# Kernel optimization log

Hardware: AMD Instinct MI355X
Metric: run time of the kernel (lower is better)

Reference implementation:

```python
import jax, jax.numpy as jnp
import numpy as np

B = 64          # graphs per batch
NP = 512        # nodes per graph (equal-sized graphs)
N = B * NP      # total nodes
E = 1_048_576   # total edges (avg degree 32)
F_IN, H, K, OUT = 16, 128, 2, 2
BN_EPS = 1e-5
EPS = 1e-15


def setup_inputs() -> dict:
    key = jax.random.key(0)
    ks = jax.random.split(key, 12)
    node_feature = jax.random.normal(ks[0], (N, F_IN), jnp.float32)
    # edges constrained to stay within each graph of NP nodes
    g = jax.random.randint(ks[1], (E,), 0, B)
    src = g * NP + jax.random.randint(ks[2], (E,), 0, NP)
    dst = g * NP + jax.random.randint(ks[3], (E,), 0, NP)
    edge_index = jnp.stack([src, dst]).astype(jnp.int32)
    edge_feature = jax.random.uniform(ks[4], (E, 1), jnp.float32)
    batch = (jnp.arange(N, dtype=jnp.int32) // NP)

    def lin(k, i, o):
        return (jax.random.normal(k, (i, o), jnp.float32) / np.sqrt(i)).astype(jnp.float32)

    params = dict(
        W_pre=lin(ks[5], F_IN, H), b_pre=jnp.zeros((H,), jnp.float32),
        W1_rel=lin(ks[6], H, H), b1_rel=jnp.zeros((H,), jnp.float32), W1_root=lin(ks[7], H, H),
        g1=jnp.ones((H,), jnp.float32), be1=jnp.zeros((H,), jnp.float32),
        W2_rel=lin(ks[8], H, H), b2_rel=jnp.zeros((H,), jnp.float32), W2_root=lin(ks[9], H, H),
        g2=jnp.ones((H,), jnp.float32), be2=jnp.zeros((H,), jnp.float32),
        W_pool=lin(ks[10], H, K), b_pool=jnp.zeros((K,), jnp.float32),
        W_post=lin(ks[11], 2 * H, OUT), b_post=jnp.zeros((OUT,), jnp.float32),
    )
    return dict(node_feature=node_feature, edge_index=edge_index,
                edge_feature=edge_feature, batch=batch, **params)


def _graph_conv(x, src, dst, ew, W_rel, b_rel, W_root):
    # PyG GraphConv: out = lin_rel(sum_{j->i} w_e * x_j) + lin_root(x_i)
    msg = x[src] * ew                       # [E, H] gather + scale
    agg = jnp.zeros_like(x).at[dst].add(msg)  # scatter-add to targets
    return agg @ W_rel + b_rel + x @ W_root


def _bn(x, g, b):
    # BatchNorm1d in training mode: batch statistics over nodes (biased var)
    mu = x.mean(0)
    var = jnp.mean((x - mu) ** 2, axis=0)
    return (x - mu) * jax.lax.rsqrt(var + BN_EPS) * g + b


def reference(node_feature, edge_index, edge_feature, batch,
              W_pre, b_pre, W1_rel, b1_rel, W1_root, g1, be1,
              W2_rel, b2_rel, W2_root, g2, be2,
              W_pool, b_pool, W_post, b_post):
    src, dst = edge_index[0], edge_index[1]
    x = node_feature @ W_pre + b_pre
    x = jax.nn.relu(_bn(_graph_conv(x, src, dst, edge_feature, W1_rel, b1_rel, W1_root), g1, be1))
    x = jax.nn.relu(_bn(_graph_conv(x, src, dst, edge_feature, W2_rel, b2_rel, W2_root), g2, be2))
    # dropout p=0.0 -> identity

    # to_dense_batch: equal-sized sorted graphs -> reshape; mask is all-ones
    xd = x.reshape(B, NP, H)
    # to_dense_adj: scatter edge weights into [B, NP, NP]
    gid, ls, ld = src // NP, src % NP, dst % NP
    adj = jnp.zeros((B, NP, NP), jnp.float32).at[gid, ls, ld].add(edge_feature[:, 0])

    # dense_mincut_pool
    s = jax.nn.softmax(xd @ W_pool + b_pool, axis=-1)          # [B, NP, K]
    out = jnp.einsum('bnk,bnh->bkh', s, xd)                     # [B, K, H]
    out_adj = jnp.einsum('bnk,bnm,bml->bkl', s, adj, s)         # [B, K, K]

    mincut_num = jnp.trace(out_adj, axis1=1, axis2=2)
    d_flat = adj.sum(-1)                                        # [B, NP]
    den_mat = jnp.einsum('bnk,bn,bnl->bkl', s, d_flat, s)
    mincut_den = jnp.trace(den_mat, axis1=1, axis2=2)
    mc_loss = jnp.mean(-(mincut_num / mincut_den))

    ss = jnp.einsum('bnk,bnl->bkl', s, s)                       # [B, K, K]
    ss_n = jnp.linalg.norm(ss, axis=(-2, -1), keepdims=True)
    i_s = jnp.eye(K, dtype=ss.dtype)
    o_loss = jnp.mean(jnp.linalg.norm(ss / ss_n - i_s / jnp.sqrt(jnp.float32(K)), axis=(-2, -1)))

    h = jax.nn.relu(out).reshape(B, K * H)
    logits = h @ W_post + b_post
    return (logits, mc_loss, o_loss)
```

## Files before the change

### kernel.cpp

```cpp
#include <hip/hip_runtime.h>

#define NN 32768
#define NP 512
#define NB 64
#define NE 1048576
#define FIN 16
#define H 128
#define BN_EPS 1e-5f
#define EPB 4096
#define NBLK (NE / EPB)
#define CAPH 8704
#define NSH 32

typedef unsigned int u32;
typedef unsigned short u16;
typedef __attribute__((ext_vector_type(8))) short bf16x8;
typedef __attribute__((ext_vector_type(4))) float f32x4;

__device__ __forceinline__ u16 f2bf(float f) {
    u32 u = __float_as_uint(f);
    return (u16)((u + 0x7fffu + ((u >> 16) & 1u)) >> 16);
}
__device__ __forceinline__ float bfLo(u32 p) { return __uint_as_float(p << 16); }
__device__ __forceinline__ float bfHi(u32 p) { return __uint_as_float(p & 0xffff0000u); }

static constexpr size_t SZ_HALF   = (size_t)NN * H * 2;
static constexpr size_t OFF_X     = 0;
static constexpr size_t OFF_AGG   = OFF_X + SZ_HALF;
static constexpr size_t OFF_TMP   = OFF_AGG;
static constexpr size_t OFF_SORT  = OFF_AGG + SZ_HALF;
static constexpr size_t OFF_OFFS  = OFF_SORT + (size_t)NE * 8;
static constexpr size_t OFF_HISTG = OFF_OFFS + ((size_t)NN + 128) * 4;
static constexpr size_t OFF_STARTG= OFF_HISTG + (size_t)NBLK * NB * 4;
static constexpr size_t OFF_GBASE = OFF_STARTG + (size_t)NBLK * NB * 4;
static constexpr size_t OFF_WT1   = OFF_GBASE + 512;
static constexpr size_t OFF_WT2   = OFF_WT1 + (size_t)H * 2 * H * 2;
static constexpr size_t OFF_S     = OFF_WT2 + (size_t)H * 2 * H * 2;
static constexpr size_t OFF_GST   = OFF_S + (size_t)NN * 2 * 4;
static constexpr size_t OFF_ZERO  = OFF_GST + 1024;
static constexpr size_t OFF_NUM   = OFF_ZERO;
static constexpr size_t OFF_DEN   = OFF_NUM + 256;
static constexpr size_t OFF_BN    = OFF_DEN + 256;
static constexpr size_t SZ_BNL    = (size_t)NSH * 2 * H * 4;
static constexpr size_t OFF_POOL  = OFF_BN + 2 * SZ_BNL;
static constexpr size_t ZERO_BYTES= (OFF_POOL + (size_t)NB * 2 * H * 4) - OFF_ZERO;


__global__ __launch_bounds__(256) void k_prep(
        const float* __restrict__ nf, const float* __restrict__ Wp,
        const float* __restrict__ bp,
        const float* __restrict__ W1_rel, const float* __restrict__ W1_root,
        const float* __restrict__ W2_rel, const float* __restrict__ W2_root,
        const int* __restrict__ src,
        u16* __restrict__ x0, u16* __restrict__ WT1, u16* __restrict__ WT2,
        int* __restrict__ histG) {
    int t = threadIdx.x, bid = blockIdx.x;
    if (bid < 2048) {
        __shared__ float sW[FIN * H];
        __shared__ float sNF[16 * FIN];
        for (int i = t; i < FIN * H; i += 256) sW[i] = Wp[i];
        int n0 = bid * 16;
        sNF[t] = nf[n0 * FIN + t];
        __syncthreads();
        int col = t & 127, half = t >> 7;
        float b = bp[col];
        #pragma unroll
        for (int r = 0; r < 8; ++r) {
            int rr = half * 8 + r;
            float acc = b;
            #pragma unroll
            for (int f = 0; f < FIN; ++f) acc += sNF[rr * FIN + f] * sW[f * H + col];
            x0[(size_t)(n0 + rr) * H + col] = f2bf(acc);
        }
    } else if (bid < 2304) {
        int base = bid - 2048;
        const float* __restrict__ Wrel = (base < 128) ? W1_rel : W2_rel;
        const float* __restrict__ Wroot = (base < 128) ? W1_root : W2_root;
        u16* WT = (base < 128) ? WT1 : WT2;
        int i = (base & 127) * 256 + t;
        int c = i >> 8, k = i & 255;
        float v = (k < H) ? Wrel[k * H + c] : Wroot[(k - H) * H + c];
        WT[c * 256 + k] = f2bf(v);
    } else {
        __shared__ int h[NB];
        if (t < NB) h[t] = 0;
        __syncthreads();
        int ebase = (bid - 2304) * EPB;
        #pragma unroll
        for (int i = 0; i < EPB / 256; ++i) {
            int s = src[ebase + i * 256 + t];
            atomicAdd(&h[s >> 9], 1);
        }
        __syncthreads();
        if (t < NB) histG[(bid - 2304) * NB + t] = h[t];
    }
}

__global__ __launch_bounds__(1024) void k_scanG(const int* __restrict__ histG,
                                                int* __restrict__ startG,
                                                int* __restrict__ gbase) {
    __shared__ int csum[16][64];
    __shared__ int gpre[64];
    int t = threadIdx.x;
    int g = t & 63, c = t >> 6;
    int vals[16];
    int s = 0;
    #pragma unroll
    for (int i = 0; i < 16; ++i) {
        vals[i] = histG[(c * 16 + i) * NB + g];
        s += vals[i];
    }
    csum[c][g] = s;
    __syncthreads();
    int pre = 0;
    for (int i = 0; i < c; ++i) pre += csum[i][g];
    if (c == 0) {
        int tot = 0;
        #pragma unroll
        for (int i = 0; i < 16; ++i) tot += csum[i][g];
        int x = tot;
        #pragma unroll
        for (int o = 1; o < 64; o <<= 1) {
            int y = __shfl_up(x, o);
            if (g >= o) x += y;
        }
        gpre[g] = x - tot;
        gbase[g] = x - tot;
        if (g == 63) gbase[64] = x;
    }
    __syncthreads();
    int run = gpre[g] + pre;
    #pragma unroll
    for (int i = 0; i < 16; ++i) {
        startG[(c * 16 + i) * NB + g] = run;
        run += vals[i];
    }
}

__global__ __launch_bounds__(256) void k_scatterA(
        const int* __restrict__ src, const int* __restrict__ dst,
        const float* __restrict__ ew, const int* __restrict__ histG,
        const int* __restrict__ startG, int2* __restrict__ tmp) {
    __shared__ int lstart[NB + 1];
    __shared__ int cursor[NB];
    __shared__ int gdst[NB];
    __shared__ int2 buf[EPB];
    int t = threadIdx.x, bid = blockIdx.x;
    if (t < NB) {
        int c = histG[bid * NB + t];
        int x = c;
        #pragma unroll
        for (int o = 1; o < 64; o <<= 1) {
            int y = __shfl_up(x, o);
            if (t >= o) x += y;
        }
        lstart[t] = x - c;
        cursor[t] = x - c;
        gdst[t] = startG[bid * NB + t];
        if (t == 63) lstart[NB] = x;
    }
    __syncthreads();
    int ebase = bid * EPB;
    #pragma unroll
    for (int i = 0; i < EPB / 256; ++i) {
        int e = ebase + i * 256 + t;
        int s = src[e], d = dst[e];
        float w = ew[e];
        int g = s >> 9;
        int meta = (s & 511) | ((d & 511) << 9);
        int p = atomicAdd(&cursor[g], 1);
        buf[p] = make_int2(meta, __float_as_int(w));
    }
    __syncthreads();
    for (int i = t; i < EPB; i += 256) {
        int lo = 0;
        #pragma unroll
        for (int stp = 32; stp; stp >>= 1)
            if (lstart[lo + stp] <= i) lo += stp;
        tmp[gdst[lo] + (i - lstart[lo])] = buf[i];
    }
}

__global__ __launch_bounds__(512) void k_sortB(
        const int2* __restrict__ tmp, const int* __restrict__ gbase,
        int2* __restrict__ sorted, int* __restrict__ offs) {
    __shared__ int hist[NP];
    __shared__ int start[NP + 1];
    __shared__ int cursor[NP / 2];
    __shared__ int wsum[8];
    __shared__ int perm[CAPH];
    int t = threadIdx.x;
    int lane = t & 63, wv = t >> 6;
    int g = blockIdx.x >> 1, half = blockIdx.x & 1;
    int gbeg = gbase[g], gend = gbase[g + 1];
    int cnt = gend - gbeg;
    hist[t] = 0;
    __syncthreads();
    for (int i = t; i < cnt; i += 512) {
        int meta = tmp[gbeg + i].x;
        atomicAdd(&hist[(meta >> 9) & 511], 1);
    }
    __syncthreads();
    int c = hist[t];
    int x = c;
    #pragma unroll
    for (int o = 1; o < 64; o <<= 1) {
        int y = __shfl_up(x, o);
        if (lane >= o) x += y;
    }
    if (lane == 63) wsum[wv] = x;
    __syncthreads();
    int off = 0;
    #pragma unroll
    for (int i = 0; i < 8; ++i) off += (i < wv) ? wsum[i] : 0;
    start[t] = off + x - c;
    if (t == 511) start[NP] = off + x;
    __syncthreads();
    int h0 = half * 256;
    if (t < 256) {
        int n = h0 + t;
        offs[g * NP + n] = gbeg + start[n];
        cursor[t] = start[n];
    }
    if (blockIdx.x == 0 && t == 0) offs[NN] = NE;
    __syncthreads();
    int ha = start[h0];
    int hb = half ? cnt : start[256];
    for (int i = t; i < cnt; i += 512) {
        int meta = tmp[gbeg + i].x;
        int d = (meta >> 9) & 511;
        if ((d >> 8) == half) {
            int p = atomicAdd(&cursor[d - h0], 1);
            perm[p - ha] = i;
        }
    }
    __syncthreads();
    for (int o = ha + t; o < hb; o += 512) {
        sorted[gbeg + o] = tmp[gbeg + perm[o - ha]];
    }
}

__global__ __launch_bounds__(256) void k_agg(const u16* __restrict__ x,
        const int* __restrict__ offs, const int2* __restrict__ rec,
        u16* __restrict__ agg) {
    int wv = threadIdx.x >> 6, lane = threadIdx.x & 63;
    int b = blockIdx.x;
    int swz = (b & 7) * (NN / 8 / 4) + (b >> 3);
    int node = swz * 4 + wv;
    int sbase = node & ~(NP - 1);
    const u16* xg = x + (size_t)sbase * H;
    int beg = offs[node], end = offs[node + 1];
    float a0 = 0.f, a1 = 0.f, b0 = 0.f, b1 = 0.f;
    int j = beg;
    for (; j + 8 <= end; j += 8) {
        int2 r0 = rec[j], r1 = rec[j + 1], r2 = rec[j + 2], r3 = rec[j + 3];
        int2 r4 = rec[j + 4], r5 = rec[j + 5], r6 = rec[j + 6], r7 = rec[j + 7];
        u32 p0 = *(const u32*)(xg + (size_t)(r0.x & 511) * H + 2 * lane);
        u32 p1 = *(const u32*)(xg + (size_t)(r1.x & 511) * H + 2 * lane);
        u32 p2 = *(const u32*)(xg + (size_t)(r2.x & 511) * H + 2 * lane);
        u32 p3 = *(const u32*)(xg + (size_t)(r3.x & 511) * H + 2 * lane);
        u32 p4 = *(const u32*)(xg + (size_t)(r4.x & 511) * H + 2 * lane);
        u32 p5 = *(const u32*)(xg + (size_t)(r5.x & 511) * H + 2 * lane);
        u32 p6 = *(const u32*)(xg + (size_t)(r6.x & 511) * H + 2 * lane);
        u32 p7 = *(const u32*)(xg + (size_t)(r7.x & 511) * H + 2 * lane);
        float w0 = __int_as_float(r0.y), w1 = __int_as_float(r1.y);
        float w2 = __int_as_float(r2.y), w3 = __int_as_float(r3.y);
        float w4 = __int_as_float(r4.y), w5 = __int_as_float(r5.y);
        float w6 = __int_as_float(r6.y), w7 = __int_as_float(r7.y);
        a0 += w0 * bfLo(p0); a1 += w0 * bfHi(p0);
        b0 += w1 * bfLo(p1); b1 += w1 * bfHi(p1);
        a0 += w2 * bfLo(p2); a1 += w2 * bfHi(p2);
        b0 += w3 * bfLo(p3); b1 += w3 * bfHi(p3);
        a0 += w4 * bfLo(p4); a1 += w4 * bfHi(p4);
        b0 += w5 * bfLo(p5); b1 += w5 * bfHi(p5);
        a0 += w6 * bfLo(p6); a1 += w6 * bfHi(p6);
        b0 += w7 * bfLo(p7); b1 += w7 * bfHi(p7);
    }
    for (; j + 2 <= end; j += 2) {
        int2 r0 = rec[j], r1 = rec[j + 1];
        u32 p0 = *(const u32*)(xg + (size_t)(r0.x & 511) * H + 2 * lane);
        u32 p1 = *(const u32*)(xg + (size_t)(r1.x & 511) * H + 2 * lane);
        float w0 = __int_as_float(r0.y), w1 = __int_as_float(r1.y);
        a0 += w0 * bfLo(p0); a1 += w0 * bfHi(p0);
        b0 += w1 * bfLo(p1); b1 += w1 * bfHi(p1);
    }
    if (j < end) {
        int2 r = rec[j];
        u32 p = *(const u32*)(xg + (size_t)(r.x & 511) * H + 2 * lane);
        float w = __int_as_float(r.y);
        a0 += w * bfLo(p); a1 += w * bfHi(p);
    }
    a0 += b0; a1 += b1;
    u32 packed = (u32)f2bf(a0) | ((u32)f2bf(a1) << 16);
    *(u32*)(agg + (size_t)node * H + 2 * lane) = packed;
}

__global__ __launch_bounds__(256) void k_gemm(
        const u16* __restrict__ Amat, const u16* Xmat,
        const u16* __restrict__ WT, const float* __restrict__ brel,
        u16* Y, float* __restrict__ bn_base) {
    __shared__ u16 sWT[128][264];
    __shared__ float colS[128], colQ[128];
    int tid = threadIdx.x;
    int w = tid >> 6, lane = tid & 63;
    int lr = lane & 15, lg = lane >> 4;
    int row0 = blockIdx.x * 64;
    int myrow = row0 + w * 16 + lr;

    bf16x8 af[8];
    const u16* pa = Amat + (size_t)myrow * H + lg * 8;
    const u16* px = Xmat + (size_t)myrow * H + lg * 8;
    #pragma unroll
    for (int kt = 0; kt < 4; ++kt) af[kt] = *(const bf16x8*)(pa + kt * 32);
    #pragma unroll
    for (int kt = 0; kt < 4; ++kt) af[4 + kt] = *(const bf16x8*)(px + kt * 32);

    for (int i = tid; i < 128 * 32; i += 256) {
        int r = i >> 5, c = i & 31;
        *(uint4*)&sWT[r][c * 8] = *(const uint4*)(WT + r * 256 + c * 8);
    }
    if (tid < 128) { colS[tid] = 0.f; colQ[tid] = 0.f; }
    __syncthreads();

    f32x4 acc[8];
    #pragma unroll
    for (int nt = 0; nt < 8; ++nt) acc[nt] = (f32x4){0.f, 0.f, 0.f, 0.f};

    #pragma unroll
    for (int kt = 0; kt < 8; ++kt) {
        #pragma unroll
        for (int nt = 0; nt < 8; ++nt) {
            bf16x8 bf = *(const bf16x8*)&sWT[nt * 16 + lr][kt * 32 + lg * 8];
            acc[nt] = __builtin_amdgcn_mfma_f32_16x16x32_bf16(af[kt], bf, acc[nt], 0, 0, 0);
        }
    }

    float cs[8], cq[8];
    #pragma unroll
    for (int nt = 0; nt < 8; ++nt) {
        int col = nt * 16 + lr;
        float bias = brel[col];
        float s = 0.f, q = 0.f;
        #pragma unroll
        for (int j = 0; j < 4; ++j) {
            float v = acc[nt][j] + bias;
            int row = row0 + w * 16 + lg * 4 + j;
            Y[(size_t)row * H + col] = f2bf(v);
            s += v; q += v * v;
        }
        cs[nt] = s; cq[nt] = q;
    }
    #pragma unroll
    for (int nt = 0; nt < 8; ++nt) {
        cs[nt] += __shfl_xor(cs[nt], 16); cs[nt] += __shfl_xor(cs[nt], 32);
        cq[nt] += __shfl_xor(cq[nt], 16); cq[nt] += __shfl_xor(cq[nt], 32);
    }
    if (lg == 0) {
        #pragma unroll
        for (int nt = 0; nt < 8; ++nt) {
            atomicAdd(&colS[nt * 16 + lr], cs[nt]);
            atomicAdd(&colQ[nt * 16 + lr], cq[nt]);
        }
    }
    __syncthreads();
    if (tid < 128) {
        int sh = blockIdx.x & (NSH - 1);
        atomicAdd(&bn_base[(sh * 2 + 0) * H + tid], colS[tid]);
        atomicAdd(&bn_base[(sh * 2 + 1) * H + tid], colQ[tid]);
    }
}

__global__ __launch_bounds__(256) void k_bnrelu(u16* __restrict__ y,
        const float* __restrict__ bn_base, const float* __restrict__ g,
        const float* __restrict__ be) {
    __shared__ float scL[H], shL[H];
    int t = threadIdx.x;
    if (t < H) {
        float su = 0.f, sq = 0.f;
        #pragma unroll
        for (int sh = 0; sh < NSH; ++sh) {
            su += bn_base[(sh * 2 + 0) * H + t];
            sq += bn_base[(sh * 2 + 1) * H + t];
        }
        float mu = su * (1.f / NN);
        float var = sq * (1.f / NN) - mu * mu;
        float sc = rsqrtf(var + BN_EPS) * g[t];
        scL[t] = sc;
        shL[t] = be[t] - mu * sc;
    }
    __syncthreads();
    #pragma unroll
    for (int it = 0; it < 4; ++it) {
        int idx = blockIdx.x * 1024 + it * 256 + t;
        int c = (idx & 15) * 8;
        uint4 u = ((const uint4*)y)[idx];
        u32 uu[4] = {u.x, u.y, u.z, u.w};
        u32 ro[4];
        #pragma unroll
        for (int p = 0; p < 4; ++p) {
            float v0 = fmaxf(fmaf(bfLo(uu[p]), scL[c + 2 * p], shL[c + 2 * p]), 0.f);
            float v1 = fmaxf(fmaf(bfHi(uu[p]), scL[c + 2 * p + 1], shL[c + 2 * p + 1]), 0.f);
            ro[p] = (u32)f2bf(v0) | ((u32)f2bf(v1) << 16);
        }
        uint4 o; o.x = ro[0]; o.y = ro[1]; o.z = ro[2]; o.w = ro[3];
        ((uint4*)y)[idx] = o;
    }
}

__global__ __launch_bounds__(256) void k_bnrelu_s(u16* __restrict__ y,
        const float* __restrict__ bn_base, const float* __restrict__ g,
        const float* __restrict__ be, const float* __restrict__ Wp,
        const float* __restrict__ bp, float* __restrict__ s,
        float* __restrict__ pool) {
    __shared__ float scL[H], shL[H];
    __shared__ float poolL[256];
    int t = threadIdx.x;
    if (t < H) {
        float su = 0.f, sq = 0.f;
        #pragma unroll
        for (int sh = 0; sh < NSH; ++sh) {
            su += bn_base[(sh * 2 + 0) * H + t];
            sq += bn_base[(sh * 2 + 1) * H + t];
        }
        float mu = su * (1.f / NN);
        float var = sq * (1.f / NN) - mu * mu;
        float sc = rsqrtf(var + BN_EPS) * g[t];
        scL[t] = sc;
        shL[t] = be[t] - mu * sc;
    }
    poolL[t] = 0.f;
    __syncthreads();
    int graph = blockIdx.x >> 3;
    int c = (t & 15) * 8;
    float pa0[8], pa1[8];
    #pragma unroll
    for (int j = 0; j < 8; ++j) { pa0[j] = 0.f; pa1[j] = 0.f; }
    #pragma unroll
    for (int it = 0; it < 4; ++it) {
        int idx = blockIdx.x * 1024 + it * 256 + t;
        uint4 u = ((const uint4*)y)[idx];
        u32 uu[4] = {u.x, u.y, u.z, u.w};
        u32 ro[4];
        float v[8];
        #pragma unroll
        for (int p = 0; p < 4; ++p) {
            v[2 * p] = fmaxf(fmaf(bfLo(uu[p]), scL[c + 2 * p], shL[c + 2 * p]), 0.f);
            v[2 * p + 1] = fmaxf(fmaf(bfHi(uu[p]), scL[c + 2 * p + 1], shL[c + 2 * p + 1]), 0.f);
            ro[p] = (u32)f2bf(v[2 * p]) | ((u32)f2bf(v[2 * p + 1]) << 16);
        }
        uint4 o; o.x = ro[0]; o.y = ro[1]; o.z = ro[2]; o.w = ro[3];
        ((uint4*)y)[idx] = o;
        float z0 = 0.f, z1 = 0.f;
        #pragma unroll
        for (int j = 0; j < 8; ++j) {
            z0 += v[j] * Wp[(c + j) * 2];
            z1 += v[j] * Wp[(c + j) * 2 + 1];
        }
        #pragma unroll
        for (int o2 = 8; o2; o2 >>= 1) { z0 += __shfl_xor(z0, o2); z1 += __shfl_xor(z1, o2); }
        z0 += bp[0]; z1 += bp[1];
        float m = fmaxf(z0, z1);
        float e0 = expf(z0 - m), e1 = expf(z1 - m);
        float inv = 1.f / (e0 + e1);
        float s0 = e0 * inv, s1 = e1 * inv;
        int row = idx >> 4;
        if ((t & 15) == 0) { s[row * 2] = s0; s[row * 2 + 1] = s1; }
        #pragma unroll
        for (int j = 0; j < 8; ++j) { pa0[j] += s0 * v[j]; pa1[j] += s1 * v[j]; }
    }
    #pragma unroll
    for (int j = 0; j < 8; ++j) {
        atomicAdd(&poolL[c + j], pa0[j]);
        atomicAdd(&poolL[128 + c + j], pa1[j]);
    }
    __syncthreads();
    if (t < 128) atomicAdd(&pool[(graph * 2 + 0) * H + t], poolL[t]);
    else atomicAdd(&pool[(graph * 2 + 1) * H + (t - 128)], poolL[t]);
}

__global__ __launch_bounds__(256) void k_edge(
        const int2* __restrict__ sorted, const int* __restrict__ gbase,
        const float* __restrict__ s, float* __restrict__ num,
        float* __restrict__ den, float* __restrict__ gst) {
    __shared__ float2 sl[NP];
    __shared__ float ln[4], ld2[4];
    int t = threadIdx.x;
    int g = blockIdx.x >> 2, q = blockIdx.x & 3;
    int gbeg = gbase[g], gend = gbase[g + 1];
    for (int i = t; i < NP; i += 256) sl[i] = ((const float2*)s)[g * NP + i];
    __syncthreads();
    float an = 0.f, ad = 0.f;
    int cnt = gend - gbeg;
    int q0 = gbeg + (cnt * q) / 4, q1 = gbeg + (cnt * (q + 1)) / 4;
    for (int i = q0 + t; i < q1; i += 256) {
        int2 r = sorted[i];
        float w = __int_as_float(r.y);
        float2 ss = sl[r.x & 511];
        float2 sd = sl[(r.x >> 9) & 511];
        an += w * (ss.x * sd.x + ss.y * sd.y);
        ad += w * (ss.x * ss.x + ss.y * ss.y);
    }
    for (int o = 32; o; o >>= 1) { an += __shfl_down(an, o); ad += __shfl_down(ad, o); }
    if ((t & 63) == 0) { ln[t >> 6] = an; ld2[t >> 6] = ad; }
    __syncthreads();
    if (t == 0) {
        atomicAdd(&num[g], ln[0] + ln[1] + ln[2] + ln[3]);
        atomicAdd(&den[g], ld2[0] + ld2[1] + ld2[2] + ld2[3]);
    }
    if (q == 0) {
        float p00 = 0.f, p01 = 0.f, p11 = 0.f;
        for (int i = t; i < NP; i += 256) {
            float2 sv = sl[i];
            p00 += sv.x * sv.x;
            p01 += sv.x * sv.y;
            p11 += sv.y * sv.y;
        }
        for (int o = 32; o; o >>= 1) {
            p00 += __shfl_down(p00, o);
            p01 += __shfl_down(p01, o);
            p11 += __shfl_down(p11, o);
        }
        __shared__ float tp[3][4];
        if ((t & 63) == 0) {
            int w = t >> 6;
            tp[0][w] = p00; tp[1][w] = p01; tp[2][w] = p11;
        }
        __syncthreads();
        if (t == 0) {
            gst[g] = tp[0][0] + tp[0][1] + tp[0][2] + tp[0][3];
            gst[NB + g] = tp[1][0] + tp[1][1] + tp[1][2] + tp[1][3];
            gst[2 * NB + g] = tp[2][0] + tp[2][1] + tp[2][2] + tp[2][3];
        }
    }
}

__global__ void k_logits_losses(const float* __restrict__ pool, const float* __restrict__ Wpost,
                                const float* __restrict__ bpost, const float* __restrict__ num,
                                const float* __restrict__ den, const float* __restrict__ gst,
                                float* __restrict__ out) {
    int t = threadIdx.x;
    if (blockIdx.x < 64) {
        int b = blockIdx.x;
        float v = pool[b * 256 + t];
        v = v > 0.f ? v : 0.f;
        float p0 = v * Wpost[t * 2], p1 = v * Wpost[t * 2 + 1];
        for (int o = 32; o; o >>= 1) { p0 += __shfl_down(p0, o); p1 += __shfl_down(p1, o); }
        __shared__ float t0[4], t1[4];
        if ((t & 63) == 0) { t0[t >> 6] = p0; t1[t >> 6] = p1; }
        __syncthreads();
        if (t == 0) {
            out[b * 2] = t0[0] + t0[1] + t0[2] + t0[3] + bpost[0];
            out[b * 2 + 1] = t1[0] + t1[1] + t1[2] + t1[3] + bpost[1];
        }
    } else if (t < 64) {
        float s00 = gst[t], s01 = gst[NB + t], s11 = gst[2 * NB + t];
        float mc = -(num[t] / den[t]);
        float nrm = sqrtf(s00 * s00 + 2.f * s01 * s01 + s11 * s11);
        const float a = 0.70710678118654752440f;
        float d00 = s00 / nrm - a, d01 = s01 / nrm, d11 = s11 / nrm - a;
        float ol = sqrtf(d00 * d00 + 2.f * d01 * d01 + d11 * d11);
        for (int o = 32; o; o >>= 1) { mc += __shfl_down(mc, o); ol += __shfl_down(ol, o); }
        if (t == 0) {
            out[NB * 2] = mc * (1.f / NB);
            out[NB * 2 + 1] = ol * (1.f / NB);
        }
    }
}

extern "C" void kernel_launch(void* const* d_in, const int* in_sizes, int n_in,
                              void* d_out, int out_size, void* d_ws, size_t ws_size,
                              hipStream_t stream) {
    const float* nf     = (const float*)d_in[0];
    const int*   ei     = (const int*)d_in[1];
    const float* ew     = (const float*)d_in[2];
    const float* W_pre  = (const float*)d_in[4];
    const float* b_pre  = (const float*)d_in[5];
    const float* W1_rel = (const float*)d_in[6];
    const float* b1_rel = (const float*)d_in[7];
    const float* W1_root= (const float*)d_in[8];
    const float* g1     = (const float*)d_in[9];
    const float* be1    = (const float*)d_in[10];
    const float* W2_rel = (const float*)d_in[11];
    const float* b2_rel = (const float*)d_in[12];
    const float* W2_root= (const float*)d_in[13];
    const float* g2     = (const float*)d_in[14];
    const float* be2    = (const float*)d_in[15];
    const float* W_pool = (const float*)d_in[16];
    const float* b_pool = (const float*)d_in[17];
    const float* W_post = (const float*)d_in[18];
    const float* b_post = (const float*)d_in[19];

    char* ws = (char*)d_ws;
    u16*   bufX   = (u16*)(ws + OFF_X);
    u16*   bufAgg = (u16*)(ws + OFF_AGG);
    int2*  tmp    = (int2*)(ws + OFF_TMP);
    int2*  sorted = (int2*)(ws + OFF_SORT);
    int*   offs   = (int*)(ws + OFF_OFFS);
    int*   histG  = (int*)(ws + OFF_HISTG);
    int*   startG = (int*)(ws + OFF_STARTG);
    int*   gbase  = (int*)(ws + OFF_GBASE);
    u16*   WT1    = (u16*)(ws + OFF_WT1);
    u16*   WT2    = (u16*)(ws + OFF_WT2);
    float* sarr   = (float*)(ws + OFF_S);
    float* gst    = (float*)(ws + OFF_GST);
    float* numA   = (float*)(ws + OFF_NUM);
    float* denA   = (float*)(ws + OFF_DEN);
    float* bn     = (float*)(ws + OFF_BN);
    float* pool   = (float*)(ws + OFF_POOL);
    float* outF   = (float*)d_out;

    const int* srcA = ei;
    const int* dstA = ei + NE;
    float* bn1 = bn;
    float* bn2 = (float*)(ws + OFF_BN + SZ_BNL);

    hipMemsetAsync(ws + OFF_ZERO, 0, ZERO_BYTES, stream);

    k_prep<<<2560, 256, 0, stream>>>(nf, W_pre, b_pre, W1_rel, W1_root,
                                     W2_rel, W2_root, srcA, bufX, WT1, WT2, histG);
    k_scanG<<<1, 1024, 0, stream>>>(histG, startG, gbase);
    k_scatterA<<<NBLK, 256, 0, stream>>>(srcA, dstA, ew, histG, startG, tmp);
    k_sortB<<<2 * NB, 512, 0, stream>>>(tmp, gbase, sorted, offs);

    k_agg<<<NN / 4, 256, 0, stream>>>(bufX, offs, sorted, bufAgg);
    k_gemm<<<NN / 64, 256, 0, stream>>>(bufAgg, bufX, WT1, b1_rel, bufX, bn1);
    k_bnrelu<<<512, 256, 0, stream>>>(bufX, bn1, g1, be1);

    k_agg<<<NN / 4, 256, 0, stream>>>(bufX, offs, sorted, bufAgg);
    k_gemm<<<NN / 64, 256, 0, stream>>>(bufAgg, bufX, WT2, b2_rel, bufX, bn2);
    k_bnrelu_s<<<512, 256, 0, stream>>>(bufX, bn2, g2, be2, W_pool, b_pool, sarr, pool);

    k_edge<<<256, 256, 0, stream>>>(sorted, gbase, sarr, numA, denA, gst);
    k_logits_losses<<<NB + 1, 256, 0, stream>>>(pool, W_post, b_post, numA, denA, gst, outF);
}
```

Before: 280.0 us.

## Fuse aggregation with GEMM, fold BN-ReLU into next layer, merge tail kernels

Aggregation and the rel/root GEMM now run in one kernel that keeps the aggregated tile in shared memory instead of writing it to global memory. The first BatchNorm+ReLU is applied on the fly while the second layer gathers its inputs, which removes the separate normalisation pass. The edge-loss and logits kernels are merged, with a last-block atomic counter computing the final losses. Costs: BN+ReLU is recomputed for every gathered neighbour, the weight tile is loaded in two halves with extra barriers, and fewer nodes are processed per wave, which may reduce occupancy and latency hiding during the gather.

```diff
diff --git a/kernel.cpp b/kernel.cpp
--- a/kernel.cpp
+++ b/kernel.cpp
@@ -10,7 +10,7 @@
 #define EPB 4096
 #define NBLK (NE / EPB)
 #define CAPH 8704
-#define NSH 32
+#define NSH 16
 
 typedef unsigned int u32;
 typedef unsigned short u16;
@@ -23,12 +23,13 @@
 }
 __device__ __forceinline__ float bfLo(u32 p) { return __uint_as_float(p << 16); }
 __device__ __forceinline__ float bfHi(u32 p) { return __uint_as_float(p & 0xffff0000u); }
+__device__ __forceinline__ float b2f(u16 v) { return __uint_as_float((u32)v << 16); }
 
 static constexpr size_t SZ_HALF   = (size_t)NN * H * 2;
 static constexpr size_t OFF_X     = 0;
-static constexpr size_t OFF_AGG   = OFF_X + SZ_HALF;
-static constexpr size_t OFF_TMP   = OFF_AGG;
-static constexpr size_t OFF_SORT  = OFF_AGG + SZ_HALF;
+static constexpr size_t OFF_TMP   = OFF_X + SZ_HALF;
+static constexpr size_t OFF_Y     = OFF_TMP;
+static constexpr size_t OFF_SORT  = OFF_TMP + (size_t)NE * 8;
 static constexpr size_t OFF_OFFS  = OFF_SORT + (size_t)NE * 8;
 static constexpr size_t OFF_HISTG = OFF_OFFS + ((size_t)NN + 128) * 4;
 static constexpr size_t OFF_STARTG= OFF_HISTG + (size_t)NBLK * NB * 4;
@@ -36,11 +37,12 @@
 static constexpr size_t OFF_WT1   = OFF_GBASE + 512;
 static constexpr size_t OFF_WT2   = OFF_WT1 + (size_t)H * 2 * H * 2;
 static constexpr size_t OFF_S     = OFF_WT2 + (size_t)H * 2 * H * 2;
-static constexpr size_t OFF_GST   = OFF_S + (size_t)NN * 2 * 4;
-static constexpr size_t OFF_ZERO  = OFF_GST + 1024;
+static constexpr size_t OFF_ZERO  = OFF_S + (size_t)NN * 2 * 4;
 static constexpr size_t OFF_NUM   = OFF_ZERO;
 static constexpr size_t OFF_DEN   = OFF_NUM + 256;
-static constexpr size_t OFF_BN    = OFF_DEN + 256;
+static constexpr size_t OFF_GST   = OFF_DEN + 256;
+static constexpr size_t OFF_CTR   = OFF_GST + 1024;
+static constexpr size_t OFF_BN    = OFF_CTR + 256;
 static constexpr size_t SZ_BNL    = (size_t)NSH * 2 * H * 4;
 static constexpr size_t OFF_POOL  = OFF_BN + 2 * SZ_BNL;
 static constexpr size_t ZERO_BYTES= (OFF_POOL + (size_t)NB * 2 * H * 4) - OFF_ZERO;
@@ -240,174 +242,166 @@
     }
 }
 
-__global__ __launch_bounds__(256) void k_agg(const u16* __restrict__ x,
-        const int* __restrict__ offs, const int2* __restrict__ rec,
-        u16* __restrict__ agg) {
-    int wv = threadIdx.x >> 6, lane = threadIdx.x & 63;
-    int b = blockIdx.x;
-    int swz = (b & 7) * (NN / 8 / 4) + (b >> 3);
-    int node = swz * 4 + wv;
-    int sbase = node & ~(NP - 1);
-    const u16* xg = x + (size_t)sbase * H;
-    int beg = offs[node], end = offs[node + 1];
-    float a0 = 0.f, a1 = 0.f, b0 = 0.f, b1 = 0.f;
-    int j = beg;
-    for (; j + 8 <= end; j += 8) {
-        int2 r0 = rec[j], r1 = rec[j + 1], r2 = rec[j + 2], r3 = rec[j + 3];
-        int2 r4 = rec[j + 4], r5 = rec[j + 5], r6 = rec[j + 6], r7 = rec[j + 7];
-        u32 p0 = *(const u32*)(xg + (size_t)(r0.x & 511) * H + 2 * lane);
-        u32 p1 = *(const u32*)(xg + (size_t)(r1.x & 511) * H + 2 * lane);
-        u32 p2 = *(const u32*)(xg + (size_t)(r2.x & 511) * H + 2 * lane);
-        u32 p3 = *(const u32*)(xg + (size_t)(r3.x & 511) * H + 2 * lane);
-        u32 p4 = *(const u32*)(xg + (size_t)(r4.x & 511) * H + 2 * lane);
-        u32 p5 = *(const u32*)(xg + (size_t)(r5.x & 511) * H + 2 * lane);
-        u32 p6 = *(const u32*)(xg + (size_t)(r6.x & 511) * H + 2 * lane);
-        u32 p7 = *(const u32*)(xg + (size_t)(r7.x & 511) * H + 2 * lane);
-        float w0 = __int_as_float(r0.y), w1 = __int_as_float(r1.y);
-        float w2 = __int_as_float(r2.y), w3 = __int_as_float(r3.y);
-        float w4 = __int_as_float(r4.y), w5 = __int_as_float(r5.y);
-        float w6 = __int_as_float(r6.y), w7 = __int_as_float(r7.y);
-        a0 += w0 * bfLo(p0); a1 += w0 * bfHi(p0);
-        b0 += w1 * bfLo(p1); b1 += w1 * bfHi(p1);
-        a0 += w2 * bfLo(p2); a1 += w2 * bfHi(p2);
-        b0 += w3 * bfLo(p3); b1 += w3 * bfHi(p3);
-        a0 += w4 * bfLo(p4); a1 += w4 * bfHi(p4);
-        b0 += w5 * bfLo(p5); b1 += w5 * bfHi(p5);
-        a0 += w6 * bfLo(p6); a1 += w6 * bfHi(p6);
-        b0 += w7 * bfLo(p7); b1 += w7 * bfHi(p7);
-    }
-    for (; j + 2 <= end; j += 2) {
-        int2 r0 = rec[j], r1 = rec[j + 1];
-        u32 p0 = *(const u32*)(xg + (size_t)(r0.x & 511) * H + 2 * lane);
-        u32 p1 = *(const u32*)(xg + (size_t)(r1.x & 511) * H + 2 * lane);
-        float w0 = __int_as_float(r0.y), w1 = __int_as_float(r1.y);
-        a0 += w0 * bfLo(p0); a1 += w0 * bfHi(p0);
-        b0 += w1 * bfLo(p1); b1 += w1 * bfHi(p1);
-    }
-    if (j < end) {
-        int2 r = rec[j];
-        u32 p = *(const u32*)(xg + (size_t)(r.x & 511) * H + 2 * lane);
-        float w = __int_as_float(r.y);
-        a0 += w * bfLo(p); a1 += w * bfHi(p);
-    }
-    a0 += b0; a1 += b1;
-    u32 packed = (u32)f2bf(a0) | ((u32)f2bf(a1) << 16);
-    *(u32*)(agg + (size_t)node * H + 2 * lane) = packed;
-}
-
-__global__ __launch_bounds__(256) void k_gemm(
-        const u16* __restrict__ Amat, const u16* Xmat,
-        const u16* __restrict__ WT, const float* __restrict__ brel,
-        u16* Y, float* __restrict__ bn_base) {
-    __shared__ u16 sWT[128][264];
+template<int APPLY_BN>
+__global__ __launch_bounds__(256, 3) void k_ag(
+        const u16* __restrict__ X, const int* __restrict__ offs,
+        const int2* __restrict__ rec, const u16* __restrict__ WT,
+        const float* __restrict__ brel,
+        const float* __restrict__ bn_prev, const float* __restrict__ gprev,
+        const float* __restrict__ beprev,
+        u16* __restrict__ Y, float* __restrict__ bn_out) {
+    __shared__ u16 sAgg[64][136];
+    __shared__ u16 sWT[64][264];
     __shared__ float colS[128], colQ[128];
-    int tid = threadIdx.x;
-    int w = tid >> 6, lane = tid & 63;
+    __shared__ float scL[128], shL[128];
+    int t = threadIdx.x, b = blockIdx.x;
+    int chunk = (b & 7) * 64 + (b >> 3);
+    int row0 = chunk * 64;
+    int sbase = row0 & ~(NP - 1);
+
+    if (APPLY_BN) {
+        if (t < 128) {
+            float su = 0.f, sq = 0.f;
+            #pragma unroll
+            for (int sh = 0; sh < NSH; ++sh) {
+                su += bn_prev[(sh * 2 + 0) * H + t];
+                sq += bn_prev[(sh * 2 + 1) * H + t];
+            }
+            float mu = su * (1.f / NN);
+            float var = sq * (1.f / NN) - mu * mu;
+            float sc = rsqrtf(var + BN_EPS) * gprev[t];
+            scL[t] = sc;
+            shL[t] = beprev[t] - mu * sc;
+        }
+        __syncthreads();
+    }
+
+    {
+        int wv = t >> 6, lane = t & 63;
+        const u16* xg = X + (size_t)sbase * H;
+        float sc0 = 0.f, sc1 = 0.f, sh0 = 0.f, sh1 = 0.f;
+        if (APPLY_BN) {
+            sc0 = scL[2 * lane]; sc1 = scL[2 * lane + 1];
+            sh0 = shL[2 * lane]; sh1 = shL[2 * lane + 1];
+        }
+        for (int r = wv; r < 64; r += 4) {
+            int node = row0 + r;
+            int beg = offs[node], end = offs[node + 1];
+            float a0 = 0.f, a1 = 0.f, c0 = 0.f, c1 = 0.f;
+            int j = beg;
+            for (; j + 4 <= end; j += 4) {
+                int2 r0 = rec[j], r1 = rec[j + 1], r2 = rec[j + 2], r3 = rec[j + 3];
+                u32 p0 = *(const u32*)(xg + (size_t)(r0.x & 511) * H + 2 * lane);
+                u32 p1 = *(const u32*)(xg + (size_t)(r1.x & 511) * H + 2 * lane);
+                u32 p2 = *(const u32*)(xg + (size_t)(r2.x & 511) * H + 2 * lane);
+                u32 p3 = *(const u32*)(xg + (size_t)(r3.x & 511) * H + 2 * lane);
+                float w0 = __int_as_float(r0.y), w1 = __int_as_float(r1.y);
+                float w2 = __int_as_float(r2.y), w3 = __int_as_float(r3.y);
+                float v00 = bfLo(p0), v01 = bfHi(p0), v10 = bfLo(p1), v11 = bfHi(p1);
+                float v20 = bfLo(p2), v21 = bfHi(p2), v30 = bfLo(p3), v31 = bfHi(p3);
+                if (APPLY_BN) {
+                    v00 = fmaxf(fmaf(v00, sc0, sh0), 0.f); v01 = fmaxf(fmaf(v01, sc1, sh1), 0.f);
+                    v10 = fmaxf(fmaf(v10, sc0, sh0), 0.f); v11 = fmaxf(fmaf(v11, sc1, sh1), 0.f);
+                    v20 = fmaxf(fmaf(v20, sc0, sh0), 0.f); v21 = fmaxf(fmaf(v21, sc1, sh1), 0.f);
+                    v30 = fmaxf(fmaf(v30, sc0, sh0), 0.f); v31 = fmaxf(fmaf(v31, sc1, sh1), 0.f);
+                }
+                a0 += w0 * v00; a1 += w0 * v01;
+                c0 += w1 * v10; c1 += w1 * v11;
+                a0 += w2 * v20; a1 += w2 * v21;
+                c0 += w3 * v30; c1 += w3 * v31;
+            }
+            for (; j < end; ++j) {
+                int2 r = rec[j];
+                u32 p = *(const u32*)(xg + (size_t)(r.x & 511) * H + 2 * lane);
+                float w = __int_as_float(r.y);
+                float v0 = bfLo(p), v1 = bfHi(p);
+                if (APPLY_BN) {
+                    v0 = fmaxf(fmaf(v0, sc0, sh0), 0.f);
+                    v1 = fmaxf(fmaf(v1, sc1, sh1), 0.f);
+                }
+                a0 += w * v0; a1 += w * v1;
+            }
+            a0 += c0; a1 += c1;
+            *(u32*)&sAgg[r][2 * lane] = (u32)f2bf(a0) | ((u32)f2bf(a1) << 16);
+        }
+    }
+    if (t < 128) { colS[t] = 0.f; colQ[t] = 0.f; }
+    __syncthreads();
+
+    int w = t >> 6, lane = t & 63;
     int lr = lane & 15, lg = lane >> 4;
-    int row0 = blockIdx.x * 64;
-    int myrow = row0 + w * 16 + lr;
-
+    int myrl = w * 16 + lr;
     bf16x8 af[8];
-    const u16* pa = Amat + (size_t)myrow * H + lg * 8;
-    const u16* px = Xmat + (size_t)myrow * H + lg * 8;
-    #pragma unroll
-    for (int kt = 0; kt < 4; ++kt) af[kt] = *(const bf16x8*)(pa + kt * 32);
-    #pragma unroll
-    for (int kt = 0; kt < 4; ++kt) af[4 + kt] = *(const bf16x8*)(px + kt * 32);
-
-    for (int i = tid; i < 128 * 32; i += 256) {
-        int r = i >> 5, c = i & 31;
-        *(uint4*)&sWT[r][c * 8] = *(const uint4*)(WT + r * 256 + c * 8);
-    }
-    if (tid < 128) { colS[tid] = 0.f; colQ[tid] = 0.f; }
-    __syncthreads();
-
-    f32x4 acc[8];
-    #pragma unroll
-    for (int nt = 0; nt < 8; ++nt) acc[nt] = (f32x4){0.f, 0.f, 0.f, 0.f};
-
-    #pragma unroll
-    for (int kt = 0; kt < 8; ++kt) {
-        #pragma unroll
-        for (int nt = 0; nt < 8; ++nt) {
-            bf16x8 bf = *(const bf16x8*)&sWT[nt * 16 + lr][kt * 32 + lg * 8];
-            acc[nt] = __builtin_amdgcn_mfma_f32_16x16x32_bf16(af[kt], bf, acc[nt], 0, 0, 0);
-        }
-    }
-
-    float cs[8], cq[8];
-    #pragma unroll
-    for (int nt = 0; nt < 8; ++nt) {
-        int col = nt * 16 + lr;
-        float bias = brel[col];
-        float s = 0.f, q = 0.f;
-        #pragma unroll
-        for (int j = 0; j < 4; ++j) {
-            float v = acc[nt][j] + bias;
-            int row = row0 + w * 16 + lg * 4 + j;
-            Y[(size_t)row * H + col] = f2bf(v);
-            s += v; q += v * v;
-        }
-        cs[nt] = s; cq[nt] = q;
-    }
-    #pragma unroll
-    for (int nt = 0; nt < 8; ++nt) {
-        cs[nt] += __shfl_xor(cs[nt], 16); cs[nt] += __shfl_xor(cs[nt], 32);
-        cq[nt] += __shfl_xor(cq[nt], 16); cq[nt] += __shfl_xor(cq[nt], 32);
-    }
-    if (lg == 0) {
-        #pragma unroll
-        for (int nt = 0; nt < 8; ++nt) {
-            atomicAdd(&colS[nt * 16 + lr], cs[nt]);
-            atomicAdd(&colQ[nt * 16 + lr], cq[nt]);
-        }
-    }
-    __syncthreads();
-    if (tid < 128) {
-        int sh = blockIdx.x & (NSH - 1);
-        atomicAdd(&bn_base[(sh * 2 + 0) * H + tid], colS[tid]);
-        atomicAdd(&bn_base[(sh * 2 + 1) * H + tid], colQ[tid]);
-    }
-}
-
-__global__ __launch_bounds__(256) void k_bnrelu(u16* __restrict__ y,
-        const float* __restrict__ bn_base, const float* __restrict__ g,
-        const float* __restrict__ be) {
-    __shared__ float scL[H], shL[H];
-    int t = threadIdx.x;
-    if (t < H) {
-        float su = 0.f, sq = 0.f;
-        #pragma unroll
-        for (int sh = 0; sh < NSH; ++sh) {
-            su += bn_base[(sh * 2 + 0) * H + t];
-            sq += bn_base[(sh * 2 + 1) * H + t];
-        }
-        float mu = su * (1.f / NN);
-        float var = sq * (1.f / NN) - mu * mu;
-        float sc = rsqrtf(var + BN_EPS) * g[t];
-        scL[t] = sc;
-        shL[t] = be[t] - mu * sc;
-    }
-    __syncthreads();
-    #pragma unroll
-    for (int it = 0; it < 4; ++it) {
-        int idx = blockIdx.x * 1024 + it * 256 + t;
-        int c = (idx & 15) * 8;
-        uint4 u = ((const uint4*)y)[idx];
-        u32 uu[4] = {u.x, u.y, u.z, u.w};
-        u32 ro[4];
-        #pragma unroll
-        for (int p = 0; p < 4; ++p) {
-            float v0 = fmaxf(fmaf(bfLo(uu[p]), scL[c + 2 * p], shL[c + 2 * p]), 0.f);
-            float v1 = fmaxf(fmaf(bfHi(uu[p]), scL[c + 2 * p + 1], shL[c + 2 * p + 1]), 0.f);
-            ro[p] = (u32)f2bf(v0) | ((u32)f2bf(v1) << 16);
-        }
-        uint4 o; o.x = ro[0]; o.y = ro[1]; o.z = ro[2]; o.w = ro[3];
-        ((uint4*)y)[idx] = o;
-    }
-}
-
-__global__ __launch_bounds__(256) void k_bnrelu_s(u16* __restrict__ y,
+    #pragma unroll
+    for (int kt = 0; kt < 4; ++kt)
+        af[kt] = *(const bf16x8*)&sAgg[myrl][kt * 32 + lg * 8];
+    const u16* px = X + (size_t)(row0 + myrl) * H + lg * 8;
+    #pragma unroll
+    for (int kt = 0; kt < 4; ++kt) {
+        bf16x8 rx = *(const bf16x8*)(px + kt * 32);
+        if (APPLY_BN) {
+            bf16x8 o;
+            #pragma unroll
+            for (int j = 0; j < 8; ++j) {
+                int cc = kt * 32 + lg * 8 + j;
+                float v = fmaxf(fmaf(b2f((u16)rx[j]), scL[cc], shL[cc]), 0.f);
+                o[j] = (short)f2bf(v);
+            }
+            af[4 + kt] = o;
+        } else {
+            af[4 + kt] = rx;
+        }
+    }
+
+    #pragma unroll
+    for (int colh = 0; colh < 2; ++colh) {
+        int col0 = colh * 64;
+        __syncthreads();
+        for (int i = t; i < 64 * 32; i += 256) {
+            int r = i >> 5, c = i & 31;
+            *(uint4*)&sWT[r][c * 8] = *(const uint4*)(WT + (size_t)(col0 + r) * 256 + c * 8);
+        }
+        __syncthreads();
+        f32x4 acc[4];
+        #pragma unroll
+        for (int nt = 0; nt < 4; ++nt) acc[nt] = (f32x4){0.f, 0.f, 0.f, 0.f};
+        #pragma unroll
+        for (int kt = 0; kt < 8; ++kt) {
+            #pragma unroll
+            for (int nt = 0; nt < 4; ++nt) {
+                bf16x8 bf = *(const bf16x8*)&sWT[nt * 16 + lr][kt * 32 + lg * 8];
+                acc[nt] = __builtin_amdgcn_mfma_f32_16x16x32_bf16(af[kt], bf, acc[nt], 0, 0, 0);
+            }
+        }
+        #pragma unroll
+        for (int nt = 0; nt < 4; ++nt) {
+            int col = col0 + nt * 16 + lr;
+            float bias = brel[col];
+            float s = 0.f, q = 0.f;
+            #pragma unroll
+            for (int j = 0; j < 4; ++j) {
+                float v = acc[nt][j] + bias;
+                int row = row0 + w * 16 + lg * 4 + j;
+                Y[(size_t)row * H + col] = f2bf(v);
+                s += v; q += v * v;
+            }
+            s += __shfl_xor(s, 16); s += __shfl_xor(s, 32);
+            q += __shfl_xor(q, 16); q += __shfl_xor(q, 32);
+            if (lg == 0) {
+                atomicAdd(&colS[col], s);
+                atomicAdd(&colQ[col], q);
+            }
+        }
+    }
+    __syncthreads();
+    if (t < 128) {
+        int sh = b & (NSH - 1);
+        atomicAdd(&bn_out[(sh * 2 + 0) * H + t], colS[t]);
+        atomicAdd(&bn_out[(sh * 2 + 1) * H + t], colQ[t]);
+    }
+}
+
+__global__ __launch_bounds__(256) void k_bnrelu_s(const u16* __restrict__ y,
         const float* __restrict__ bn_base, const float* __restrict__ g,
         const float* __restrict__ be, const float* __restrict__ Wp,
         const float* __restrict__ bp, float* __restrict__ s,
@@ -440,16 +434,12 @@
         int idx = blockIdx.x * 1024 + it * 256 + t;
         uint4 u = ((const uint4*)y)[idx];
         u32 uu[4] = {u.x, u.y, u.z, u.w};
-        u32 ro[4];
         float v[8];
         #pragma unroll
         for (int p = 0; p < 4; ++p) {
             v[2 * p] = fmaxf(fmaf(bfLo(uu[p]), scL[c + 2 * p], shL[c + 2 * p]), 0.f);
             v[2 * p + 1] = fmaxf(fmaf(bfHi(uu[p]), scL[c + 2 * p + 1], shL[c + 2 * p + 1]), 0.f);
-            ro[p] = (u32)f2bf(v[2 * p]) | ((u32)f2bf(v[2 * p + 1]) << 16);
-        }
-        uint4 o; o.x = ro[0]; o.y = ro[1]; o.z = ro[2]; o.w = ro[3];
-        ((uint4*)y)[idx] = o;
+        }
         float z0 = 0.f, z1 = 0.f;
         #pragma unroll
         for (int j = 0; j < 8; ++j) {
@@ -478,14 +468,33 @@
     else atomicAdd(&pool[(graph * 2 + 1) * H + (t - 128)], poolL[t]);
 }
 
-__global__ __launch_bounds__(256) void k_edge(
+__global__ __launch_bounds__(256) void k_edge_logits(
         const int2* __restrict__ sorted, const int* __restrict__ gbase,
-        const float* __restrict__ s, float* __restrict__ num,
-        float* __restrict__ den, float* __restrict__ gst) {
+        const float* __restrict__ s, const float* __restrict__ pool,
+        const float* __restrict__ Wpost, const float* __restrict__ bpost,
+        float* __restrict__ num, float* __restrict__ den,
+        float* __restrict__ gst, int* __restrict__ ctr,
+        float* __restrict__ out) {
+    int t = threadIdx.x, b = blockIdx.x;
+    if (b >= 256) {
+        int gb = b - 256;
+        float v = pool[gb * 256 + t];
+        v = v > 0.f ? v : 0.f;
+        float p0 = v * Wpost[t * 2], p1 = v * Wpost[t * 2 + 1];
+        for (int o = 32; o; o >>= 1) { p0 += __shfl_down(p0, o); p1 += __shfl_down(p1, o); }
+        __shared__ float t0[4], t1[4];
+        if ((t & 63) == 0) { t0[t >> 6] = p0; t1[t >> 6] = p1; }
+        __syncthreads();
+        if (t == 0) {
+            out[gb * 2] = t0[0] + t0[1] + t0[2] + t0[3] + bpost[0];
+            out[gb * 2 + 1] = t1[0] + t1[1] + t1[2] + t1[3] + bpost[1];
+        }
+        return;
+    }
     __shared__ float2 sl[NP];
     __shared__ float ln[4], ld2[4];
-    int t = threadIdx.x;
-    int g = blockIdx.x >> 2, q = blockIdx.x & 3;
+    __shared__ int lastFlag;
+    int g = b >> 2, q = b & 3;
     int gbeg = gbase[g], gend = gbase[g + 1];
     for (int i = t; i < NP; i += 256) sl[i] = ((const float2*)s)[g * NP + i];
     __syncthreads();
@@ -527,34 +536,24 @@
         }
         __syncthreads();
         if (t == 0) {
-            gst[g] = tp[0][0] + tp[0][1] + tp[0][2] + tp[0][3];
-            gst[NB + g] = tp[1][0] + tp[1][1] + tp[1][2] + tp[1][3];
-            gst[2 * NB + g] = tp[2][0] + tp[2][1] + tp[2][2] + tp[2][3];
-        }
-    }
-}
-
-__global__ void k_logits_losses(const float* __restrict__ pool, const float* __restrict__ Wpost,
-                                const float* __restrict__ bpost, const float* __restrict__ num,
-                                const float* __restrict__ den, const float* __restrict__ gst,
-                                float* __restrict__ out) {
-    int t = threadIdx.x;
-    if (blockIdx.x < 64) {
-        int b = blockIdx.x;
-        float v = pool[b * 256 + t];
-        v = v > 0.f ? v : 0.f;
-        float p0 = v * Wpost[t * 2], p1 = v * Wpost[t * 2 + 1];
-        for (int o = 32; o; o >>= 1) { p0 += __shfl_down(p0, o); p1 += __shfl_down(p1, o); }
-        __shared__ float t0[4], t1[4];
-        if ((t & 63) == 0) { t0[t >> 6] = p0; t1[t >> 6] = p1; }
-        __syncthreads();
-        if (t == 0) {
-            out[b * 2] = t0[0] + t0[1] + t0[2] + t0[3] + bpost[0];
-            out[b * 2 + 1] = t1[0] + t1[1] + t1[2] + t1[3] + bpost[1];
-        }
-    } else if (t < 64) {
-        float s00 = gst[t], s01 = gst[NB + t], s11 = gst[2 * NB + t];
-        float mc = -(num[t] / den[t]);
+            atomicAdd(&gst[g], tp[0][0] + tp[0][1] + tp[0][2] + tp[0][3]);
+            atomicAdd(&gst[NB + g], tp[1][0] + tp[1][1] + tp[1][2] + tp[1][3]);
+            atomicAdd(&gst[2 * NB + g], tp[2][0] + tp[2][1] + tp[2][2] + tp[2][3]);
+        }
+    }
+    if (t == 0) {
+        __threadfence();
+        int old = atomicAdd(ctr, 1);
+        lastFlag = (old == 255);
+    }
+    __syncthreads();
+    if (lastFlag && t < 64) {
+        float nv = atomicAdd(&num[t], 0.f);
+        float dv = atomicAdd(&den[t], 0.f);
+        float s00 = atomicAdd(&gst[t], 0.f);
+        float s01 = atomicAdd(&gst[NB + t], 0.f);
+        float s11 = atomicAdd(&gst[2 * NB + t], 0.f);
+        float mc = -(nv / dv);
         float nrm = sqrtf(s00 * s00 + 2.f * s01 * s01 + s11 * s11);
         const float a = 0.70710678118654752440f;
         float d00 = s00 / nrm - a, d01 = s01 / nrm, d11 = s11 / nrm - a;
@@ -592,7 +591,7 @@
 
     char* ws = (char*)d_ws;
     u16*   bufX   = (u16*)(ws + OFF_X);
-    u16*   bufAgg = (u16*)(ws + OFF_AGG);
+    u16*   bufY   = (u16*)(ws + OFF_Y);
     int2*  tmp    = (int2*)(ws + OFF_TMP);
     int2*  sorted = (int2*)(ws + OFF_SORT);
     int*   offs   = (int*)(ws + OFF_OFFS);
@@ -605,6 +604,7 @@
     float* gst    = (float*)(ws + OFF_GST);
     float* numA   = (float*)(ws + OFF_NUM);
     float* denA   = (float*)(ws + OFF_DEN);
+    int*   ctr    = (int*)(ws + OFF_CTR);
     float* bn     = (float*)(ws + OFF_BN);
     float* pool   = (float*)(ws + OFF_POOL);
     float* outF   = (float*)d_out;
@@ -622,14 +622,11 @@
     k_scatterA<<<NBLK, 256, 0, stream>>>(srcA, dstA, ew, histG, startG, tmp);
     k_sortB<<<2 * NB, 512, 0, stream>>>(tmp, gbase, sorted, offs);
 
-    k_agg<<<NN / 4, 256, 0, stream>>>(bufX, offs, sorted, bufAgg);
-    k_gemm<<<NN / 64, 256, 0, stream>>>(bufAgg, bufX, WT1, b1_rel, bufX, bn1);
-    k_bnrelu<<<512, 256, 0, stream>>>(bufX, bn1, g1, be1);
-
-    k_agg<<<NN / 4, 256, 0, stream>>>(bufX, offs, sorted, bufAgg);
-    k_gemm<<<NN / 64, 256, 0, stream>>>(bufAgg, bufX, WT2, b2_rel, bufX, bn2);
+    k_ag<0><<<NN / 64, 256, 0, stream>>>(bufX, offs, sorted, WT1, b1_rel,
+                                         nullptr, nullptr, nullptr, bufY, bn1);
+    k_ag<1><<<NN / 64, 256, 0, stream>>>(bufY, offs, sorted, WT2, b2_rel,
+                                         bn1, g1, be1, bufX, bn2);
     k_bnrelu_s<<<512, 256, 0, stream>>>(bufX, bn2, g2, be2, W_pool, b_pool, sarr, pool);
-
-    k_edge<<<256, 256, 0, stream>>>(sorted, gbase, sarr, numA, denA, gst);
-    k_logits_losses<<<NB + 1, 256, 0, stream>>>(pool, W_post, b_post, numA, denA, gst, outF);
-}
+    k_edge_logits<<<320, 256, 0, stream>>>(sorted, gbase, sarr, pool, W_post, b_post,
+                                           numA, denA, gst, ctr, outF);
+}
```

After: 320.9 us. 1.15x slower.
